# Performance work log

Measured on AMD Instinct MI355X. Metric: run time of the kernel, lower is better.

## Reference

```python
import jax, jax.numpy as jnp
import numpy as np
import math

IN_SIZE = 512
OUT_SIZE = 512
N_HEADS = 8
D_K = OUT_SIZE // N_HEADS  # 64
N_NTYPES = 4
N_ETYPES = 8
MAX_LEN = 240
E = 150000


def _sinusoid_table():
    # RelTemporalEncoding fixed (non-trainable) embedding table [MAX_LEN, IN_SIZE]
    position = np.arange(0.0, MAX_LEN, dtype=np.float64)[:, None]
    div_term = np.exp(np.arange(0, IN_SIZE, 2, dtype=np.float64) * -(math.log(10000.0) / IN_SIZE))
    emb = np.zeros((MAX_LEN, IN_SIZE), dtype=np.float64)
    emb[:, 0::2] = np.sin(position * div_term) / IN_SIZE ** 0.5
    emb[:, 1::2] = np.cos(position * div_term) / IN_SIZE ** 0.5
    return jnp.asarray(emb, dtype=jnp.float32)


def typed_linear(x, types, W, b=None):
    """x: [E, ..., in], types: int[E], W: [T, out, in], b: [T, out] or None.
    Small fixed loop over T types with masked accumulation (avoids gathering a
    huge [E, out, in] weight tensor)."""
    out = jnp.zeros(x.shape[:-1] + (W.shape[1],), x.dtype)
    t_exp = types.reshape((-1,) + (1,) * (x.ndim - 1))
    for t in range(W.shape[0]):
        y = jnp.einsum('...i,oi->...o', x, W[t])
        if b is not None:
            y = y + b[t]
        out = out + jnp.where(t_exp == t, y, jnp.zeros((), x.dtype))
    return out


def setup_inputs() -> dict:
    key = jax.random.key(0)
    ks = jax.random.split(key, 12)
    xavier = lambda k, shape, fan_in, fan_out: jax.random.uniform(
        k, shape, jnp.float32, -1.0, 1.0) * math.sqrt(6.0 / (fan_in + fan_out))
    inp = {
        'h_s': jax.random.normal(ks[0], (E, IN_SIZE), jnp.float32),
        'Q_t': jax.random.normal(ks[1], (E, N_HEADS, D_K), jnp.float32),
        'etype': jax.random.randint(ks[2], (E,), 0, N_ETYPES),
        'tau_s': jax.random.randint(ks[3], (E,), 0, N_NTYPES),
        'dt': jax.random.randint(ks[4], (E,), 0, MAX_LEN),
        # RelTemporalEncoding params
        'emb': _sinusoid_table(),  # fixed, non-trainable
        'lin_W': xavier(ks[5], (IN_SIZE, IN_SIZE), IN_SIZE, IN_SIZE),
        'lin_b': jnp.zeros((IN_SIZE,), jnp.float32),
        # TypedLinear params (xavier_uniform like the torch code)
        'K_W': xavier(ks[6], (N_NTYPES, OUT_SIZE, IN_SIZE), IN_SIZE, OUT_SIZE),
        'K_b': jnp.zeros((N_NTYPES, OUT_SIZE), jnp.float32),
        'V_W': xavier(ks[7], (N_NTYPES, OUT_SIZE, IN_SIZE), IN_SIZE, OUT_SIZE),
        'V_b': jnp.zeros((N_NTYPES, OUT_SIZE), jnp.float32),
        'Watt_W': xavier(ks[8], (N_ETYPES, D_K, D_K), D_K, D_K),
        'Wmsg_W': xavier(ks[9], (N_ETYPES, D_K, D_K), D_K, D_K),
        'mu': jnp.ones((N_ETYPES, N_HEADS), jnp.float32),
    }
    return inp


def reference(h_s, Q_t, etype, tau_s, dt, emb, lin_W, lin_b,
              K_W, K_b, V_W, V_b, Watt_W, Wmsg_W, mu):
    n_edges = h_s.shape[0]
    # RelTemporalEncoding: x + Linear(emb[t])
    h_hat = h_s + emb[dt] @ lin_W.T + lin_b  # [E, in]
    # Typed K/V projections by source node type
    K_s = typed_linear(h_hat, tau_s, K_W, K_b).reshape(n_edges, N_HEADS, D_K)
    V_s = typed_linear(h_hat, tau_s, V_W, V_b).reshape(n_edges, N_HEADS, D_K)
    # Typed per-edge-type transforms
    M = typed_linear(V_s, etype, Wmsg_W)          # [E, H, d_k]
    att_head_k = typed_linear(K_s, etype, Watt_W)  # [E, H, d_k]
    att_head = (Q_t * att_head_k).sum(-1)          # [E, H]
    att_head = att_head * mu[etype] / D_K ** 0.5
    return att_head, M
```

## Files before the change

### kernel.cpp

```cpp
#include <hip/hip_runtime.h>
#include <hip/hip_bf16.h>
#include <stdint.h>

#define E_N 150000
#define IN 512
#define MAXLEN 240

#define PT 150528
#define PE 150528
#define NTILE_T 1176

typedef __attribute__((ext_vector_type(8))) short short8;
typedef __attribute__((ext_vector_type(4))) short short4v;
typedef __attribute__((ext_vector_type(4))) float f32x4;

#define OFF_R    0UL
#define OFF_WC   491520UL
#define OFF_BIAS 4685824UL
#define OFF_CNT  4702208UL
#define OFF_PT   4702464UL
#define OFF_PE   5304576UL
#define OFF_KS   5906688UL

static __device__ __forceinline__ short f2bf(float f) {
  union { float f; uint32_t u; } v; v.f = f;
  uint32_t u = v.u;
  uint32_t r = (u + 0x7fffu + ((u >> 16) & 1u)) >> 16;
  return (short)r;
}

__global__ __launch_bounds__(256) void k_rte(const float* __restrict__ emb,
    const float* __restrict__ linW, const float* __restrict__ linB,
    float* __restrict__ R) {
  __shared__ float x[IN];
  int p = blockIdx.x;
  for (int i = threadIdx.x; i < IN; i += 256) x[i] = emb[p * IN + i];
  __syncthreads();
  for (int o = threadIdx.x; o < IN; o += 256) {
    const float* w = linW + (long)o * IN;
    float s = 0.f;
#pragma unroll 4
    for (int k = 0; k < IN; k += 4) {
      float4 wv = *(const float4*)(w + k);
      s += wv.x * x[k] + wv.y * x[k + 1] + wv.z * x[k + 2] + wv.w * x[k + 3];
    }
    R[p * IN + o] = s + linB[o];
  }
}

__global__ __launch_bounds__(256) void k_cvtw(const float* __restrict__ KW,
    const float* __restrict__ VW, short* __restrict__ Wc) {
  long idx = ((long)blockIdx.x * 256 + threadIdx.x) * 4;
  int t = (int)(idx >> 19);
  int rem = (int)(idx & ((1 << 19) - 1));
  int o = rem >> 9;
  int k = rem & 511;
  const float* src = (o < 512) ? (KW + ((long)(t * 512 + o) * 512) + k)
                               : (VW + ((long)(t * 512 + (o - 512)) * 512) + k);
  float4 v = *(const float4*)src;
  short4v b;
  b.x = f2bf(v.x); b.y = f2bf(v.y); b.z = f2bf(v.z); b.w = f2bf(v.w);
  *(short4v*)(Wc + idx) = b;
}

__global__ __launch_bounds__(256) void k_cvtb(const float* __restrict__ Kb,
    const float* __restrict__ Vb, float* __restrict__ biasC) {
  int idx = blockIdx.x * 256 + threadIdx.x;
  int t = idx >> 10;
  int o = idx & 1023;
  biasC[idx] = (o < 512) ? Kb[t * 512 + o] : Vb[t * 512 + (o - 512)];
}

__global__ __launch_bounds__(256) void k_hist(const int* __restrict__ tau,
    const int* __restrict__ et, int* __restrict__ cnt) {
  __shared__ int l[12];
  if (threadIdx.x < 12) l[threadIdx.x] = 0;
  __syncthreads();
  int e = blockIdx.x * 256 + threadIdx.x;
  if (e < E_N) {
    atomicAdd(&l[tau[e]], 1);
    atomicAdd(&l[4 + et[e]], 1);
  }
  __syncthreads();
  if (threadIdx.x < 12) atomicAdd(&cnt[threadIdx.x], l[threadIdx.x]);
}

__global__ void k_bases(int* c) {
  int b = 0;
  for (int t = 0; t < 4; t++) { c[12 + t] = b; b += ((c[t] + 127) >> 7) << 7; }
  b = 0;
  for (int g = 0; g < 8; g++) { c[16 + g] = b; b += ((c[4 + g] + 63) >> 6) << 6; }
  for (int i = 24; i < 36; i++) c[i] = 0;
}

__global__ __launch_bounds__(256) void k_scatter(const int* __restrict__ tau,
    const int* __restrict__ et, int* __restrict__ c,
    int* __restrict__ permT, int* __restrict__ permE) {
  __shared__ int lc[12], lbase[12];
  if (threadIdx.x < 12) lc[threadIdx.x] = 0;
  __syncthreads();
  int e = blockIdx.x * 256 + threadIdx.x;
  bool v = e < E_N;
  int t = 0, g = 0, pt = 0, pe = 0;
  if (v) {
    t = tau[e]; g = et[e];
    pt = atomicAdd(&lc[t], 1);
    pe = atomicAdd(&lc[4 + g], 1);
  }
  __syncthreads();
  if (threadIdx.x < 12) {
    int n = lc[threadIdx.x];
    int base = 0;
    if (n > 0) {
      if (threadIdx.x < 4) base = atomicAdd(&c[24 + threadIdx.x], n);
      else                 base = atomicAdd(&c[28 + (threadIdx.x - 4)], n);
    }
    lbase[threadIdx.x] = base;
  }
  __syncthreads();
  if (v) {
    permT[c[12 + t] + lbase[t] + pt] = e;
    permE[c[16 + g] + lbase[4 + g] + pe] = e;
  }
}

__global__ __launch_bounds__(256) void k_hhat(const float* __restrict__ hs,
    const float* __restrict__ R, const int* __restrict__ dt,
    char* __restrict__ out) {
  int tid = threadIdx.x;
  long e = (long)blockIdx.x * 16 + (tid >> 4);
  int sub = tid & 15;
  const float* hp = hs + e * 512 + sub * 32;
  const float* rp = R + (long)dt[e] * 512 + sub * 32;
  short* op = (short*)(out + e * 2048) + sub * 32;
#pragma unroll
  for (int j = 0; j < 4; j++) {
    float4 h0 = *(const float4*)(hp + j * 8);
    float4 h1 = *(const float4*)(hp + j * 8 + 4);
    float4 r0 = *(const float4*)(rp + j * 8);
    float4 r1 = *(const float4*)(rp + j * 8 + 4);
    short8 o;
    o[0] = f2bf(h0.x + r0.x); o[1] = f2bf(h0.y + r0.y);
    o[2] = f2bf(h0.z + r0.z); o[3] = f2bf(h0.w + r0.w);
    o[4] = f2bf(h1.x + r1.x); o[5] = f2bf(h1.y + r1.y);
    o[6] = f2bf(h1.z + r1.z); o[7] = f2bf(h1.w + r1.w);
    *(short8*)(op + j * 8) = o;
  }
}

__global__ __launch_bounds__(256, 4) void k_gemm(
    const char* __restrict__ hhat,
    const int* __restrict__ tau,
    const short* __restrict__ Wc, const float* __restrict__ biasC,
    const int* __restrict__ perm,
    short* __restrict__ Ks, float* Mout) {
  __shared__ short sA[4096];
  __shared__ short sB[4096];
  __shared__ int eRow[128];
  __shared__ int metaT;
  int tid = threadIdx.x;
  int l = (blockIdx.x & 7) * NTILE_T + (blockIdx.x >> 3);
  int ttile = l >> 3, ctile = l & 7;
  int m0 = ttile * 128;
  if (tid < 128) eRow[tid] = perm[m0 + tid];
  if (tid == 0) {
    int e0 = perm[m0];
    metaT = (e0 >= 0) ? tau[e0] : -1;
  }
  __syncthreads();
  int t = metaT;
  if (t < 0) return;
  int n0 = ctile * 128;

  int lane = tid & 63;
  int w = tid >> 6;
  int wm = w >> 1, wn = w & 1;

  int rS = w * 32 + (lane >> 2);
  int cS = lane & 3;
  int e0r = eRow[rS];      if (e0r < 0) e0r = 0;
  int e1r = eRow[rS + 16]; if (e1r < 0) e1r = 0;
  int ch0 = (cS - (rS >> 1)) & 3;
  int ch1 = (cS - ((rS + 16) >> 1)) & 3;
  const char* srcA0 = hhat + (size_t)e0r * 2048 + ch0 * 16;
  const char* srcA1 = hhat + (size_t)e1r * 2048 + ch1 * 16;
  const char* wcb = (const char*)(Wc + ((size_t)t * 1024 + n0) * 512);
  const char* srcB0 = wcb + (size_t)rS * 1024 + ch0 * 16;
  const char* srcB1 = wcb + (size_t)(rS + 16) * 1024 + ch1 * 16;
  char* dA0 = (char*)sA + w * 2048;
  char* dA1 = (char*)sA + w * 2048 + 1024;
  char* dB0 = (char*)sB + w * 2048;
  char* dB1 = (char*)sB + w * 2048 + 1024;

  int aRow = wm * 64 + (lane & 15);
  int aOff = aRow * 64 + ((((lane >> 4) + (aRow >> 1)) & 3) << 4);
  int bRow = wn * 64 + (lane & 15);
  int bOff = bRow * 64 + ((((lane >> 4) + (bRow >> 1)) & 3) << 4);

  f32x4 acc[4][4] = {};
#pragma unroll
  for (int kk = 0; kk < 16; kk++) {
    __syncthreads();
    __builtin_amdgcn_global_load_lds((const uint32_t*)(srcA0 + kk * 64), (uint32_t*)dA0, 16, 0, 0);
    __builtin_amdgcn_global_load_lds((const uint32_t*)(srcA1 + kk * 64), (uint32_t*)dA1, 16, 0, 0);
    __builtin_amdgcn_global_load_lds((const uint32_t*)(srcB0 + kk * 64), (uint32_t*)dB0, 16, 0, 0);
    __builtin_amdgcn_global_load_lds((const uint32_t*)(srcB1 + kk * 64), (uint32_t*)dB1, 16, 0, 0);
    __syncthreads();
    short8 a[4], b[4];
#pragma unroll
    for (int mi = 0; mi < 4; mi++)
      a[mi] = *(const short8*)((const char*)sA + aOff + mi * 1024);
#pragma unroll
    for (int ni = 0; ni < 4; ni++)
      b[ni] = *(const short8*)((const char*)sB + bOff + ni * 1024);
#pragma unroll
    for (int mi = 0; mi < 4; mi++)
#pragma unroll
      for (int ni = 0; ni < 4; ni++)
        acc[mi][ni] = __builtin_amdgcn_mfma_f32_16x16x32_bf16(a[mi], b[ni], acc[mi][ni], 0, 0, 0);
  }

  int l15 = lane & 15;
  int rbase = (lane >> 4) * 4;
  bool isK = ctile < 4;
  float bias[4];
#pragma unroll
  for (int ni = 0; ni < 4; ni++)
    bias[ni] = biasC[t * 1024 + n0 + wn * 64 + ni * 16 + l15];
#pragma unroll
  for (int mi = 0; mi < 4; mi++) {
#pragma unroll
    for (int r = 0; r < 4; r++) {
      int row = wm * 64 + mi * 16 + rbase + r;
      int e = eRow[row];
      if (e < 0) continue;
      if (isK) {
        short* kd = Ks + (size_t)e * 512 + n0 + wn * 64;
#pragma unroll
        for (int ni = 0; ni < 4; ni++)
          kd[ni * 16 + l15] = f2bf(acc[mi][ni][r] + bias[ni]);
      } else {
        short* vd = (short*)((char*)Mout + (size_t)e * 2048 + 1024) + (n0 - 512) + wn * 64;
#pragma unroll
        for (int ni = 0; ni < 4; ni++)
          vd[ni * 16 + l15] = f2bf(acc[mi][ni][r] + bias[ni]);
      }
    }
  }
}

__global__ __launch_bounds__(512, 1) void k_msg(
    const int* __restrict__ perm, const int* __restrict__ et,
    const float* __restrict__ WmsgW, float* Mout) {
  __shared__ short Wm[64][68];
  __shared__ int eArr[64];
  __shared__ int metaG;
  int tid = threadIdx.x;
  int m0 = blockIdx.x * 64;
  if (tid < 64) eArr[tid] = perm[m0 + tid];
  if (tid == 0) {
    int e0 = perm[m0];
    metaG = (e0 >= 0) ? et[e0] : -1;
  }
  __syncthreads();
  int g = metaG;
  if (g < 0) return;
  for (int i = tid; i < 4096; i += 512)
    Wm[i >> 6][i & 63] = f2bf(WmsgW[(long)g * 4096 + i]);
  __syncthreads();

  int lane = tid & 63;
  int wv = tid >> 6;
  int wvBase = wv * 64;
  int l15 = lane & 15;
  int lk8 = (lane >> 4) * 8;
  int rbase = (lane >> 4) * 4;

  short8 av[4][2];
#pragma unroll
  for (int mi = 0; mi < 4; mi++) {
    int lr = wvBase + mi * 16 + l15;
    int e = eArr[lr >> 3]; if (e < 0) e = 0;
    const short* vp = (const short*)((const char*)Mout + (size_t)e * 2048 + 1024)
                      + (lr & 7) * 64 + lk8;
    av[mi][0] = *(const short8*)vp;
    av[mi][1] = *(const short8*)(vp + 32);
  }
  short8 bm[4][2];
#pragma unroll
  for (int ni = 0; ni < 4; ni++)
#pragma unroll
    for (int kk = 0; kk < 2; kk++)
      bm[ni][kk] = *(const short8*)&Wm[ni * 16 + l15][kk * 32 + lk8];
  f32x4 accM[4][4] = {};
#pragma unroll
  for (int kk = 0; kk < 2; kk++)
#pragma unroll
    for (int mi = 0; mi < 4; mi++)
#pragma unroll
      for (int ni = 0; ni < 4; ni++)
        accM[mi][ni] = __builtin_amdgcn_mfma_f32_16x16x32_bf16(av[mi][kk], bm[ni][kk], accM[mi][ni], 0, 0, 0);
#pragma unroll
  for (int mi = 0; mi < 4; mi++) {
#pragma unroll
    for (int r = 0; r < 4; r++) {
      int lr = wvBase + mi * 16 + rbase + r;
      int e = eArr[lr >> 3];
      if (e < 0) continue;
      int h = lr & 7;
#pragma unroll
      for (int ni = 0; ni < 4; ni++)
        Mout[(long)e * 512 + h * 64 + ni * 16 + l15] = accM[mi][ni][r];
    }
  }
}

__global__ __launch_bounds__(512, 1) void k_att(
    const int* __restrict__ perm, const int* __restrict__ et,
    const float* __restrict__ WattW, const float* __restrict__ Qt,
    const float* __restrict__ mu, const short* __restrict__ Ks,
    float* __restrict__ attOut) {
  __shared__ short Wa[64][68];
  __shared__ float muL[8];
  __shared__ int eArr[64];
  __shared__ int metaG;
  int tid = threadIdx.x;
  int m0 = blockIdx.x * 64;
  if (tid < 64) eArr[tid] = perm[m0 + tid];
  if (tid == 0) {
    int e0 = perm[m0];
    metaG = (e0 >= 0) ? et[e0] : -1;
  }
  __syncthreads();
  int g = metaG;
  if (g < 0) return;
  for (int i = tid; i < 4096; i += 512)
    Wa[i >> 6][i & 63] = f2bf(WattW[(long)g * 4096 + i]);
  if (tid < 8) muL[tid] = mu[g * 8 + tid];
  __syncthreads();

  int lane = tid & 63;
  int wv = tid >> 6;
  int wvBase = wv * 64;
  int l15 = lane & 15;
  int lk8 = (lane >> 4) * 8;
  int rbase = (lane >> 4) * 4;

  short8 ak[4][2];
#pragma unroll
  for (int mi = 0; mi < 4; mi++) {
    int lr = wvBase + mi * 16 + l15;
    int e = eArr[lr >> 3]; if (e < 0) e = 0;
    const short* kp = Ks + (size_t)e * 512 + (lr & 7) * 64 + lk8;
    ak[mi][0] = *(const short8*)kp;
    ak[mi][1] = *(const short8*)(kp + 32);
  }
  short8 ba[4][2];
#pragma unroll
  for (int ni = 0; ni < 4; ni++)
#pragma unroll
    for (int kk = 0; kk < 2; kk++)
      ba[ni][kk] = *(const short8*)&Wa[ni * 16 + l15][kk * 32 + lk8];
  f32x4 accA[4][4] = {};
#pragma unroll
  for (int kk = 0; kk < 2; kk++)
#pragma unroll
    for (int mi = 0; mi < 4; mi++)
#pragma unroll
      for (int ni = 0; ni < 4; ni++)
        accA[mi][ni] = __builtin_amdgcn_mfma_f32_16x16x32_bf16(ak[mi][kk], ba[ni][kk], accA[mi][ni], 0, 0, 0);
#pragma unroll
  for (int mi = 0; mi < 4; mi++) {
#pragma unroll
    for (int r = 0; r < 4; r++) {
      int lr = wvBase + mi * 16 + rbase + r;
      int e = eArr[lr >> 3];
      if (e < 0) continue;
      int h = lr & 7;
      const float* qp = Qt + ((long)e * 8 + h) * 64 + l15;
      float s = 0.f;
#pragma unroll
      for (int ni = 0; ni < 4; ni++)
        s += qp[ni * 16] * accA[mi][ni][r];
      s += __shfl_xor(s, 1);
      s += __shfl_xor(s, 2);
      s += __shfl_xor(s, 4);
      s += __shfl_xor(s, 8);
      if (l15 == 0) attOut[(long)e * 8 + h] = s * muL[h] * 0.125f;
    }
  }
}

extern "C" void kernel_launch(void* const* d_in, const int* in_sizes, int n_in,
                              void* d_out, int out_size, void* d_ws, size_t ws_size,
                              hipStream_t stream) {
  const float* hs    = (const float*)d_in[0];
  const float* Qt    = (const float*)d_in[1];
  const int*   et    = (const int*)d_in[2];
  const int*   tau   = (const int*)d_in[3];
  const int*   dt    = (const int*)d_in[4];
  const float* emb   = (const float*)d_in[5];
  const float* linW  = (const float*)d_in[6];
  const float* linB  = (const float*)d_in[7];
  const float* KW    = (const float*)d_in[8];
  const float* Kb    = (const float*)d_in[9];
  const float* VW    = (const float*)d_in[10];
  const float* Vb    = (const float*)d_in[11];
  const float* WattW = (const float*)d_in[12];
  const float* WmsgW = (const float*)d_in[13];
  const float* mu    = (const float*)d_in[14];

  char* ws = (char*)d_ws;
  float* R     = (float*)(ws + OFF_R);
  short* Wc    = (short*)(ws + OFF_WC);
  float* biasC = (float*)(ws + OFF_BIAS);
  int*   cnt   = (int*)(ws + OFF_CNT);
  int*   permT = (int*)(ws + OFF_PT);
  int*   permE = (int*)(ws + OFF_PE);
  short* Ks    = (short*)(ws + OFF_KS);

  float* attOut = (float*)d_out;
  float* Mout   = (float*)d_out + (long)E_N * 8;

  hipMemsetAsync(cnt, 0, 64 * sizeof(int), stream);
  hipMemsetAsync(permT, 0xFF, PT * sizeof(int), stream);
  hipMemsetAsync(permE, 0xFF, PE * sizeof(int), stream);

  k_rte<<<240, 256, 0, stream>>>(emb, linW, linB, R);
  k_cvtw<<<2048, 256, 0, stream>>>(KW, VW, Wc);
  k_cvtb<<<16, 256, 0, stream>>>(Kb, Vb, biasC);
  k_hist<<<(E_N + 255) / 256, 256, 0, stream>>>(tau, et, cnt);
  k_bases<<<1, 1, 0, stream>>>(cnt);
  k_scatter<<<(E_N + 255) / 256, 256, 0, stream>>>(tau, et, cnt, permT, permE);
  k_hhat<<<E_N / 16, 256, 0, stream>>>(hs, R, dt, (char*)Mout);
  k_gemm<<<NTILE_T * 8, 256, 0, stream>>>((const char*)Mout, tau, Wc, biasC, permT, Ks, Mout);
  k_msg<<<PE / 64, 512, 0, stream>>>(permE, et, WmsgW, Mout);
  k_att<<<PE / 64, 512, 0, stream>>>(permE, et, WattW, Qt, mu, Ks, attOut);
}
```

Baseline: 693.3 us.

## Fold per-edge-type transforms into typed K/V weights and precompute temporal term

Pre-multiplies the per-edge-type Watt/Wmsg matrices into the per-node-type K/V weights, giving 32 combined (tau, etype) weight sets. Edges are bucketed by that pair. The temporal-encoding contribution is precomputed as a 240-row table per pair, so the main GEMM consumes h_s directly, converting fp32 to bf16 on the fly. The attention dot product with Q and the M store are fused into the GEMM epilogue. This removes the h_hat materialisation, the intermediate K/V buffers and the separate message and attention kernels. The cost is more padding from 32 buckets, a large RW table read per edge in the epilogue, and different rounding from bf16 combined weights.

```diff
diff --git a/kernel.cpp b/kernel.cpp
--- a/kernel.cpp
+++ b/kernel.cpp
@@ -6,21 +6,19 @@
 #define IN 512
 #define MAXLEN 240
 
-#define PT 150528
-#define PE 150528
-#define NTILE_T 1176
+#define PPERM 154112
+#define NTILE2 1204
+#define GRID_GEMM (NTILE2 * 8)
 
 typedef __attribute__((ext_vector_type(8))) short short8;
-typedef __attribute__((ext_vector_type(4))) short short4v;
 typedef __attribute__((ext_vector_type(4))) float f32x4;
 
-#define OFF_R    0UL
-#define OFF_WC   491520UL
-#define OFF_BIAS 4685824UL
-#define OFF_CNT  4702208UL
-#define OFF_PT   4702464UL
-#define OFF_PE   5304576UL
-#define OFF_KS   5906688UL
+#define OFF_RB   0UL
+#define OFF_W2   245760UL
+#define OFF_B2   33800192UL
+#define OFF_RW   33931264UL
+#define OFF_CNT  65388544UL
+#define OFF_PERM 65389056UL
 
 static __device__ __forceinline__ short f2bf(float f) {
   union { float f; uint32_t u; } v; v.f = f;
@@ -29,9 +27,15 @@
   return (short)r;
 }
 
+static __device__ __forceinline__ uint32_t pk2(float a, float b) {
+  union { __hip_bfloat162 h; uint32_t u; } v;
+  v.h = __float22bfloat162_rn(make_float2(a, b));
+  return v.u;
+}
+
 __global__ __launch_bounds__(256) void k_rte(const float* __restrict__ emb,
     const float* __restrict__ linW, const float* __restrict__ linB,
-    float* __restrict__ R) {
+    short* __restrict__ Rbf) {
   __shared__ float x[IN];
   int p = blockIdx.x;
   for (int i = threadIdx.x; i < IN; i += 256) x[i] = emb[p * IN + i];
@@ -44,147 +48,76 @@
       float4 wv = *(const float4*)(w + k);
       s += wv.x * x[k] + wv.y * x[k + 1] + wv.z * x[k + 2] + wv.w * x[k + 3];
     }
-    R[p * IN + o] = s + linB[o];
-  }
-}
-
-__global__ __launch_bounds__(256) void k_cvtw(const float* __restrict__ KW,
-    const float* __restrict__ VW, short* __restrict__ Wc) {
-  long idx = ((long)blockIdx.x * 256 + threadIdx.x) * 4;
-  int t = (int)(idx >> 19);
-  int rem = (int)(idx & ((1 << 19) - 1));
-  int o = rem >> 9;
-  int k = rem & 511;
-  const float* src = (o < 512) ? (KW + ((long)(t * 512 + o) * 512) + k)
-                               : (VW + ((long)(t * 512 + (o - 512)) * 512) + k);
-  float4 v = *(const float4*)src;
-  short4v b;
-  b.x = f2bf(v.x); b.y = f2bf(v.y); b.z = f2bf(v.z); b.w = f2bf(v.w);
-  *(short4v*)(Wc + idx) = b;
-}
-
-__global__ __launch_bounds__(256) void k_cvtb(const float* __restrict__ Kb,
-    const float* __restrict__ Vb, float* __restrict__ biasC) {
-  int idx = blockIdx.x * 256 + threadIdx.x;
-  int t = idx >> 10;
-  int o = idx & 1023;
-  biasC[idx] = (o < 512) ? Kb[t * 512 + o] : Vb[t * 512 + (o - 512)];
-}
-
-__global__ __launch_bounds__(256) void k_hist(const int* __restrict__ tau,
-    const int* __restrict__ et, int* __restrict__ cnt) {
-  __shared__ int l[12];
-  if (threadIdx.x < 12) l[threadIdx.x] = 0;
-  __syncthreads();
-  int e = blockIdx.x * 256 + threadIdx.x;
-  if (e < E_N) {
-    atomicAdd(&l[tau[e]], 1);
-    atomicAdd(&l[4 + et[e]], 1);
-  }
-  __syncthreads();
-  if (threadIdx.x < 12) atomicAdd(&cnt[threadIdx.x], l[threadIdx.x]);
-}
-
-__global__ void k_bases(int* c) {
-  int b = 0;
-  for (int t = 0; t < 4; t++) { c[12 + t] = b; b += ((c[t] + 127) >> 7) << 7; }
-  b = 0;
-  for (int g = 0; g < 8; g++) { c[16 + g] = b; b += ((c[4 + g] + 63) >> 6) << 6; }
-  for (int i = 24; i < 36; i++) c[i] = 0;
-}
-
-__global__ __launch_bounds__(256) void k_scatter(const int* __restrict__ tau,
-    const int* __restrict__ et, int* __restrict__ c,
-    int* __restrict__ permT, int* __restrict__ permE) {
-  __shared__ int lc[12], lbase[12];
-  if (threadIdx.x < 12) lc[threadIdx.x] = 0;
-  __syncthreads();
-  int e = blockIdx.x * 256 + threadIdx.x;
-  bool v = e < E_N;
-  int t = 0, g = 0, pt = 0, pe = 0;
-  if (v) {
-    t = tau[e]; g = et[e];
-    pt = atomicAdd(&lc[t], 1);
-    pe = atomicAdd(&lc[4 + g], 1);
-  }
-  __syncthreads();
-  if (threadIdx.x < 12) {
-    int n = lc[threadIdx.x];
-    int base = 0;
-    if (n > 0) {
-      if (threadIdx.x < 4) base = atomicAdd(&c[24 + threadIdx.x], n);
-      else                 base = atomicAdd(&c[28 + (threadIdx.x - 4)], n);
-    }
-    lbase[threadIdx.x] = base;
-  }
-  __syncthreads();
-  if (v) {
-    permT[c[12 + t] + lbase[t] + pt] = e;
-    permE[c[16 + g] + lbase[4 + g] + pe] = e;
-  }
-}
-
-__global__ __launch_bounds__(256) void k_hhat(const float* __restrict__ hs,
-    const float* __restrict__ R, const int* __restrict__ dt,
-    char* __restrict__ out) {
+    Rbf[p * IN + o] = f2bf(s + linB[o]);
+  }
+}
+
+__global__ __launch_bounds__(256) void k_wpair(
+    const float* __restrict__ WattW, const float* __restrict__ WmsgW,
+    const float* __restrict__ KW, const float* __restrict__ VW,
+    const float* __restrict__ Kb, const float* __restrict__ Vb,
+    short* __restrict__ W2, float* __restrict__ B2) {
+  __shared__ float Tl[64][65];
+  int blk = blockIdx.x;
+  int p = blk >> 4, s = blk & 15;
+  int t = p >> 3, g = p & 7;
+  bool kside = s < 8;
+  int h = kside ? s : s - 8;
+  const float* T = (kside ? WattW : WmsgW) + (size_t)g * 4096;
+  const float* S = (kside ? KW : VW) + ((size_t)t * 512 + h * 64) * 512;
+  const float* bsrc = (kside ? Kb : Vb) + t * 512 + h * 64;
   int tid = threadIdx.x;
-  long e = (long)blockIdx.x * 16 + (tid >> 4);
-  int sub = tid & 15;
-  const float* hp = hs + e * 512 + sub * 32;
-  const float* rp = R + (long)dt[e] * 512 + sub * 32;
-  short* op = (short*)(out + e * 2048) + sub * 32;
-#pragma unroll
-  for (int j = 0; j < 4; j++) {
-    float4 h0 = *(const float4*)(hp + j * 8);
-    float4 h1 = *(const float4*)(hp + j * 8 + 4);
-    float4 r0 = *(const float4*)(rp + j * 8);
-    float4 r1 = *(const float4*)(rp + j * 8 + 4);
-    short8 o;
-    o[0] = f2bf(h0.x + r0.x); o[1] = f2bf(h0.y + r0.y);
-    o[2] = f2bf(h0.z + r0.z); o[3] = f2bf(h0.w + r0.w);
-    o[4] = f2bf(h1.x + r1.x); o[5] = f2bf(h1.y + r1.y);
-    o[6] = f2bf(h1.z + r1.z); o[7] = f2bf(h1.w + r1.w);
-    *(short8*)(op + j * 8) = o;
-  }
-}
-
-__global__ __launch_bounds__(256, 4) void k_gemm(
-    const char* __restrict__ hhat,
-    const int* __restrict__ tau,
-    const short* __restrict__ Wc, const float* __restrict__ biasC,
-    const int* __restrict__ perm,
-    short* __restrict__ Ks, float* Mout) {
+  for (int i = tid; i < 4096; i += 256) Tl[i >> 6][i & 63] = T[i];
+  __syncthreads();
+  int op = tid & 63, iq = tid >> 6;
+  size_t obase = ((size_t)p * 1024 + (kside ? 0 : 512) + h * 64 + op) * 512;
+  for (int i8 = 0; i8 < 16; i8++) {
+    int i0 = iq * 128 + i8 * 8;
+    float a0 = 0, a1 = 0, a2 = 0, a3 = 0, a4 = 0, a5 = 0, a6 = 0, a7 = 0;
+    const float* sp0 = S + i0;
+#pragma unroll 8
+    for (int j = 0; j < 64; j++) {
+      float tv = Tl[op][j];
+      const float* sp = sp0 + j * 512;
+      float4 s0 = *(const float4*)sp;
+      float4 s1 = *(const float4*)(sp + 4);
+      a0 += tv * s0.x; a1 += tv * s0.y; a2 += tv * s0.z; a3 += tv * s0.w;
+      a4 += tv * s1.x; a5 += tv * s1.y; a6 += tv * s1.z; a7 += tv * s1.w;
+    }
+    short8 o8;
+    o8[0] = f2bf(a0); o8[1] = f2bf(a1); o8[2] = f2bf(a2); o8[3] = f2bf(a3);
+    o8[4] = f2bf(a4); o8[5] = f2bf(a5); o8[6] = f2bf(a6); o8[7] = f2bf(a7);
+    *(short8*)(W2 + obase + i0) = o8;
+  }
+  if (tid < 64) {
+    float b = 0;
+#pragma unroll 8
+    for (int j = 0; j < 64; j++) b += Tl[tid][j] * bsrc[j];
+    B2[p * 1024 + (kside ? 0 : 512) + h * 64 + tid] = b;
+  }
+}
+
+__global__ __launch_bounds__(256, 4) void k_rw2(
+    const short* __restrict__ Rbf, const short* __restrict__ W2,
+    const float* __restrict__ B2, float* __restrict__ RW) {
   __shared__ short sA[4096];
   __shared__ short sB[4096];
-  __shared__ int eRow[128];
-  __shared__ int metaT;
   int tid = threadIdx.x;
-  int l = (blockIdx.x & 7) * NTILE_T + (blockIdx.x >> 3);
-  int ttile = l >> 3, ctile = l & 7;
-  int m0 = ttile * 128;
-  if (tid < 128) eRow[tid] = perm[m0 + tid];
-  if (tid == 0) {
-    int e0 = perm[m0];
-    metaT = (e0 >= 0) ? tau[e0] : -1;
-  }
-  __syncthreads();
-  int t = metaT;
-  if (t < 0) return;
+  int bid = blockIdx.x;
+  int p = bid >> 4, rt = (bid >> 3) & 1, ctile = bid & 7;
   int n0 = ctile * 128;
-
-  int lane = tid & 63;
-  int w = tid >> 6;
-  int wm = w >> 1, wn = w & 1;
+  int r0 = rt * 128;
+
+  int lane = tid & 63, w = tid >> 6, wm = w >> 1, wn = w & 1;
 
   int rS = w * 32 + (lane >> 2);
   int cS = lane & 3;
-  int e0r = eRow[rS];      if (e0r < 0) e0r = 0;
-  int e1r = eRow[rS + 16]; if (e1r < 0) e1r = 0;
   int ch0 = (cS - (rS >> 1)) & 3;
   int ch1 = (cS - ((rS + 16) >> 1)) & 3;
-  const char* srcA0 = hhat + (size_t)e0r * 2048 + ch0 * 16;
-  const char* srcA1 = hhat + (size_t)e1r * 2048 + ch1 * 16;
-  const char* wcb = (const char*)(Wc + ((size_t)t * 1024 + n0) * 512);
+  const char* rbb = (const char*)Rbf;
+  const char* srcA0 = rbb + (size_t)(r0 + rS) * 1024 + ch0 * 16;
+  const char* srcA1 = rbb + (size_t)(r0 + rS + 16) * 1024 + ch1 * 16;
+  const char* wcb = (const char*)(W2 + ((size_t)p * 1024 + n0) * 512);
   const char* srcB0 = wcb + (size_t)rS * 1024 + ch0 * 16;
   const char* srcB1 = wcb + (size_t)(rS + 16) * 1024 + ch1 * 16;
   char* dA0 = (char*)sA + w * 2048;
@@ -222,171 +155,195 @@
 
   int l15 = lane & 15;
   int rbase = (lane >> 4) * 4;
-  bool isK = ctile < 4;
   float bias[4];
 #pragma unroll
   for (int ni = 0; ni < 4; ni++)
-    bias[ni] = biasC[t * 1024 + n0 + wn * 64 + ni * 16 + l15];
+    bias[ni] = B2[p * 1024 + n0 + wn * 64 + ni * 16 + l15];
 #pragma unroll
   for (int mi = 0; mi < 4; mi++) {
 #pragma unroll
     for (int r = 0; r < 4; r++) {
-      int row = wm * 64 + mi * 16 + rbase + r;
-      int e = eRow[row];
-      if (e < 0) continue;
-      if (isK) {
-        short* kd = Ks + (size_t)e * 512 + n0 + wn * 64;
-#pragma unroll
-        for (int ni = 0; ni < 4; ni++)
-          kd[ni * 16 + l15] = f2bf(acc[mi][ni][r] + bias[ni]);
-      } else {
-        short* vd = (short*)((char*)Mout + (size_t)e * 2048 + 1024) + (n0 - 512) + wn * 64;
-#pragma unroll
-        for (int ni = 0; ni < 4; ni++)
-          vd[ni * 16 + l15] = f2bf(acc[mi][ni][r] + bias[ni]);
-      }
-    }
-  }
-}
-
-__global__ __launch_bounds__(512, 1) void k_msg(
-    const int* __restrict__ perm, const int* __restrict__ et,
-    const float* __restrict__ WmsgW, float* Mout) {
-  __shared__ short Wm[64][68];
-  __shared__ int eArr[64];
-  __shared__ int metaG;
+      int row = r0 + wm * 64 + mi * 16 + rbase + r;
+      if (row >= MAXLEN) continue;
+      float* dst = RW + ((size_t)p * 240 + row) * 1024 + n0 + wn * 64;
+#pragma unroll
+      for (int ni = 0; ni < 4; ni++)
+        dst[ni * 16 + l15] = acc[mi][ni][r] + bias[ni];
+    }
+  }
+}
+
+__global__ __launch_bounds__(256) void k_hist(const int* __restrict__ tau,
+    const int* __restrict__ et, int* __restrict__ cnt) {
+  __shared__ int l[32];
+  if (threadIdx.x < 32) l[threadIdx.x] = 0;
+  __syncthreads();
+  int e = blockIdx.x * 256 + threadIdx.x;
+  if (e < E_N) atomicAdd(&l[tau[e] * 8 + et[e]], 1);
+  __syncthreads();
+  if (threadIdx.x < 32) atomicAdd(&cnt[threadIdx.x], l[threadIdx.x]);
+}
+
+__global__ void k_bases(int* c) {
+  int b = 0;
+  for (int p = 0; p < 32; p++) {
+    c[32 + p] = b;
+    b += ((c[p] + 127) >> 7) << 7;
+    c[64 + p] = 0;
+  }
+}
+
+__global__ __launch_bounds__(256) void k_scatter(const int* __restrict__ tau,
+    const int* __restrict__ et, int* __restrict__ c, int* __restrict__ perm) {
+  __shared__ int lc[32], lbase[32];
+  if (threadIdx.x < 32) lc[threadIdx.x] = 0;
+  __syncthreads();
+  int e = blockIdx.x * 256 + threadIdx.x;
+  bool v = e < E_N;
+  int cls = 0, pos = 0;
+  if (v) {
+    cls = tau[e] * 8 + et[e];
+    pos = atomicAdd(&lc[cls], 1);
+  }
+  __syncthreads();
+  if (threadIdx.x < 32) {
+    int n = lc[threadIdx.x];
+    lbase[threadIdx.x] = (n > 0) ? atomicAdd(&c[64 + threadIdx.x], n) : 0;
+  }
+  __syncthreads();
+  if (v) perm[c[32 + cls] + lbase[cls] + pos] = e;
+}
+
+__global__ __launch_bounds__(256, 4) void k_gemm(
+    const float* __restrict__ hs, const int* __restrict__ dt,
+    const int* __restrict__ tau, const int* __restrict__ et,
+    const short* __restrict__ W2, const float* __restrict__ RW,
+    const float* __restrict__ Qt, const float* __restrict__ mu,
+    const int* __restrict__ perm,
+    float* __restrict__ Mout, float* __restrict__ attOut) {
+  __shared__ short sA[128][40];
+  __shared__ short sB[4096];
+  __shared__ int eRow[128];
+  __shared__ int dtRow[128];
+  __shared__ int metaP;
   int tid = threadIdx.x;
-  int m0 = blockIdx.x * 64;
-  if (tid < 64) eArr[tid] = perm[m0 + tid];
+  int l = (blockIdx.x & 7) * NTILE2 + (blockIdx.x >> 3);
+  int ttile = l >> 3, ctile = l & 7;
+  int m0 = ttile * 128;
+  if (tid < 128) {
+    int e = perm[m0 + tid];
+    eRow[tid] = e;
+    dtRow[tid] = (e >= 0) ? dt[e] : 0;
+  }
   if (tid == 0) {
     int e0 = perm[m0];
-    metaG = (e0 >= 0) ? et[e0] : -1;
-  }
-  __syncthreads();
-  int g = metaG;
-  if (g < 0) return;
-  for (int i = tid; i < 4096; i += 512)
-    Wm[i >> 6][i & 63] = f2bf(WmsgW[(long)g * 4096 + i]);
-  __syncthreads();
-
-  int lane = tid & 63;
-  int wv = tid >> 6;
-  int wvBase = wv * 64;
+    metaP = (e0 >= 0) ? (tau[e0] * 8 + et[e0]) : -1;
+  }
+  __syncthreads();
+  int p = metaP;
+  if (p < 0) return;
+  int n0 = ctile * 128;
+
+  int lane = tid & 63, w = tid >> 6, wm = w >> 1, wn = w & 1;
+
+  int arow = tid >> 1;
+  int ahalf = tid & 1;
+  long aE = eRow[arow]; if (aE < 0) aE = 0;
+  const float* asrc = hs + aE * 512 + ahalf * 16;
+
+  int rS = w * 32 + (lane >> 2);
+  int cS = lane & 3;
+  int ch0 = (cS - (rS >> 1)) & 3;
+  int ch1 = (cS - ((rS + 16) >> 1)) & 3;
+  const char* wcb = (const char*)(W2 + ((size_t)p * 1024 + n0) * 512);
+  const char* srcB0 = wcb + (size_t)rS * 1024 + ch0 * 16;
+  const char* srcB1 = wcb + (size_t)(rS + 16) * 1024 + ch1 * 16;
+  char* dB0 = (char*)sB + w * 2048;
+  char* dB1 = (char*)sB + w * 2048 + 1024;
+
+  int aRowF = wm * 64 + (lane & 15);
+  int lk8 = (lane >> 4) * 8;
+  int bRow = wn * 64 + (lane & 15);
+  int bOff = bRow * 64 + ((((lane >> 4) + (bRow >> 1)) & 3) << 4);
+
+  f32x4 acc[4][4] = {};
+  float4 pf0 = *(const float4*)(asrc);
+  float4 pf1 = *(const float4*)(asrc + 4);
+  float4 pf2 = *(const float4*)(asrc + 8);
+  float4 pf3 = *(const float4*)(asrc + 12);
+#pragma unroll
+  for (int kk = 0; kk < 16; kk++) {
+    __syncthreads();
+    union { short8 s; uint32_t u[4]; } w0, w1;
+    w0.u[0] = pk2(pf0.x, pf0.y); w0.u[1] = pk2(pf0.z, pf0.w);
+    w0.u[2] = pk2(pf1.x, pf1.y); w0.u[3] = pk2(pf1.z, pf1.w);
+    w1.u[0] = pk2(pf2.x, pf2.y); w1.u[1] = pk2(pf2.z, pf2.w);
+    w1.u[2] = pk2(pf3.x, pf3.y); w1.u[3] = pk2(pf3.z, pf3.w);
+    *(short8*)&sA[arow][ahalf * 16] = w0.s;
+    *(short8*)&sA[arow][ahalf * 16 + 8] = w1.s;
+    __builtin_amdgcn_global_load_lds((const uint32_t*)(srcB0 + kk * 64), (uint32_t*)dB0, 16, 0, 0);
+    __builtin_amdgcn_global_load_lds((const uint32_t*)(srcB1 + kk * 64), (uint32_t*)dB1, 16, 0, 0);
+    if (kk < 15) {
+      const float* np = asrc + (kk + 1) * 32;
+      pf0 = *(const float4*)(np);
+      pf1 = *(const float4*)(np + 4);
+      pf2 = *(const float4*)(np + 8);
+      pf3 = *(const float4*)(np + 12);
+    }
+    __syncthreads();
+    short8 a[4], b[4];
+#pragma unroll
+    for (int mi = 0; mi < 4; mi++)
+      a[mi] = *(const short8*)&sA[aRowF + mi * 16][lk8];
+#pragma unroll
+    for (int ni = 0; ni < 4; ni++)
+      b[ni] = *(const short8*)((const char*)sB + bOff + ni * 1024);
+#pragma unroll
+    for (int mi = 0; mi < 4; mi++)
+#pragma unroll
+      for (int ni = 0; ni < 4; ni++)
+        acc[mi][ni] = __builtin_amdgcn_mfma_f32_16x16x32_bf16(a[mi], b[ni], acc[mi][ni], 0, 0, 0);
+  }
+
   int l15 = lane & 15;
-  int lk8 = (lane >> 4) * 8;
   int rbase = (lane >> 4) * 4;
-
-  short8 av[4][2];
-#pragma unroll
-  for (int mi = 0; mi < 4; mi++) {
-    int lr = wvBase + mi * 16 + l15;
-    int e = eArr[lr >> 3]; if (e < 0) e = 0;
-    const short* vp = (const short*)((const char*)Mout + (size_t)e * 2048 + 1024)
-                      + (lr & 7) * 64 + lk8;
-    av[mi][0] = *(const short8*)vp;
-    av[mi][1] = *(const short8*)(vp + 32);
-  }
-  short8 bm[4][2];
-#pragma unroll
-  for (int ni = 0; ni < 4; ni++)
-#pragma unroll
-    for (int kk = 0; kk < 2; kk++)
-      bm[ni][kk] = *(const short8*)&Wm[ni * 16 + l15][kk * 32 + lk8];
-  f32x4 accM[4][4] = {};
-#pragma unroll
-  for (int kk = 0; kk < 2; kk++)
-#pragma unroll
-    for (int mi = 0; mi < 4; mi++)
-#pragma unroll
-      for (int ni = 0; ni < 4; ni++)
-        accM[mi][ni] = __builtin_amdgcn_mfma_f32_16x16x32_bf16(av[mi][kk], bm[ni][kk], accM[mi][ni], 0, 0, 0);
-#pragma unroll
-  for (int mi = 0; mi < 4; mi++) {
-#pragma unroll
-    for (int r = 0; r < 4; r++) {
-      int lr = wvBase + mi * 16 + rbase + r;
-      int e = eArr[lr >> 3];
-      if (e < 0) continue;
-      int h = lr & 7;
-#pragma unroll
-      for (int ni = 0; ni < 4; ni++)
-        Mout[(long)e * 512 + h * 64 + ni * 16 + l15] = accM[mi][ni][r];
-    }
-  }
-}
-
-__global__ __launch_bounds__(512, 1) void k_att(
-    const int* __restrict__ perm, const int* __restrict__ et,
-    const float* __restrict__ WattW, const float* __restrict__ Qt,
-    const float* __restrict__ mu, const short* __restrict__ Ks,
-    float* __restrict__ attOut) {
-  __shared__ short Wa[64][68];
-  __shared__ float muL[8];
-  __shared__ int eArr[64];
-  __shared__ int metaG;
-  int tid = threadIdx.x;
-  int m0 = blockIdx.x * 64;
-  if (tid < 64) eArr[tid] = perm[m0 + tid];
-  if (tid == 0) {
-    int e0 = perm[m0];
-    metaG = (e0 >= 0) ? et[e0] : -1;
-  }
-  __syncthreads();
-  int g = metaG;
-  if (g < 0) return;
-  for (int i = tid; i < 4096; i += 512)
-    Wa[i >> 6][i & 63] = f2bf(WattW[(long)g * 4096 + i]);
-  if (tid < 8) muL[tid] = mu[g * 8 + tid];
-  __syncthreads();
-
-  int lane = tid & 63;
-  int wv = tid >> 6;
-  int wvBase = wv * 64;
-  int l15 = lane & 15;
-  int lk8 = (lane >> 4) * 8;
-  int rbase = (lane >> 4) * 4;
-
-  short8 ak[4][2];
-#pragma unroll
-  for (int mi = 0; mi < 4; mi++) {
-    int lr = wvBase + mi * 16 + l15;
-    int e = eArr[lr >> 3]; if (e < 0) e = 0;
-    const short* kp = Ks + (size_t)e * 512 + (lr & 7) * 64 + lk8;
-    ak[mi][0] = *(const short8*)kp;
-    ak[mi][1] = *(const short8*)(kp + 32);
-  }
-  short8 ba[4][2];
-#pragma unroll
-  for (int ni = 0; ni < 4; ni++)
-#pragma unroll
-    for (int kk = 0; kk < 2; kk++)
-      ba[ni][kk] = *(const short8*)&Wa[ni * 16 + l15][kk * 32 + lk8];
-  f32x4 accA[4][4] = {};
-#pragma unroll
-  for (int kk = 0; kk < 2; kk++)
-#pragma unroll
-    for (int mi = 0; mi < 4; mi++)
-#pragma unroll
-      for (int ni = 0; ni < 4; ni++)
-        accA[mi][ni] = __builtin_amdgcn_mfma_f32_16x16x32_bf16(ak[mi][kk], ba[ni][kk], accA[mi][ni], 0, 0, 0);
-#pragma unroll
-  for (int mi = 0; mi < 4; mi++) {
-#pragma unroll
-    for (int r = 0; r < 4; r++) {
-      int lr = wvBase + mi * 16 + rbase + r;
-      int e = eArr[lr >> 3];
-      if (e < 0) continue;
-      int h = lr & 7;
-      const float* qp = Qt + ((long)e * 8 + h) * 64 + l15;
-      float s = 0.f;
-#pragma unroll
-      for (int ni = 0; ni < 4; ni++)
-        s += qp[ni * 16] * accA[mi][ni][r];
-      s += __shfl_xor(s, 1);
-      s += __shfl_xor(s, 2);
-      s += __shfl_xor(s, 4);
-      s += __shfl_xor(s, 8);
-      if (l15 == 0) attOut[(long)e * 8 + h] = s * muL[h] * 0.125f;
+  if (ctile < 4) {
+    int h = ctile * 2 + wn;
+    float muv = mu[(p & 7) * 8 + h] * 0.125f;
+#pragma unroll
+    for (int mi = 0; mi < 4; mi++) {
+#pragma unroll
+      for (int r = 0; r < 4; r++) {
+        int row = wm * 64 + mi * 16 + rbase + r;
+        int e = eRow[row];
+        if (e < 0) continue;
+        const float* rw = RW + ((size_t)p * 240 + dtRow[row]) * 1024 + n0 + wn * 64;
+        const float* qp = Qt + (size_t)e * 512 + h * 64;
+        float s = 0.f;
+#pragma unroll
+        for (int ni = 0; ni < 4; ni++)
+          s += qp[ni * 16 + l15] * (acc[mi][ni][r] + rw[ni * 16 + l15]);
+        s += __shfl_xor(s, 1);
+        s += __shfl_xor(s, 2);
+        s += __shfl_xor(s, 4);
+        s += __shfl_xor(s, 8);
+        if (l15 == 0) attOut[(size_t)e * 8 + h] = s * muv;
+      }
+    }
+  } else {
+#pragma unroll
+    for (int mi = 0; mi < 4; mi++) {
+#pragma unroll
+      for (int r = 0; r < 4; r++) {
+        int row = wm * 64 + mi * 16 + rbase + r;
+        int e = eRow[row];
+        if (e < 0) continue;
+        const float* rw = RW + ((size_t)p * 240 + dtRow[row]) * 1024 + n0 + wn * 64;
+        float* md = Mout + (size_t)e * 512 + (n0 - 512) + wn * 64;
+#pragma unroll
+        for (int ni = 0; ni < 4; ni++)
+          md[ni * 16 + l15] = acc[mi][ni][r] + rw[ni * 16 + l15];
+      }
     }
   }
 }
@@ -411,29 +368,24 @@
   const float* mu    = (const float*)d_in[14];
 
   char* ws = (char*)d_ws;
-  float* R     = (float*)(ws + OFF_R);
-  short* Wc    = (short*)(ws + OFF_WC);
-  float* biasC = (float*)(ws + OFF_BIAS);
-  int*   cnt   = (int*)(ws + OFF_CNT);
-  int*   permT = (int*)(ws + OFF_PT);
-  int*   permE = (int*)(ws + OFF_PE);
-  short* Ks    = (short*)(ws + OFF_KS);
+  short* Rbf  = (short*)(ws + OFF_RB);
+  short* W2   = (short*)(ws + OFF_W2);
+  float* B2   = (float*)(ws + OFF_B2);
+  float* RW   = (float*)(ws + OFF_RW);
+  int*   cnt  = (int*)(ws + OFF_CNT);
+  int*   perm = (int*)(ws + OFF_PERM);
 
   float* attOut = (float*)d_out;
   float* Mout   = (float*)d_out + (long)E_N * 8;
 
-  hipMemsetAsync(cnt, 0, 64 * sizeof(int), stream);
-  hipMemsetAsync(permT, 0xFF, PT * sizeof(int), stream);
-  hipMemsetAsync(permE, 0xFF, PE * sizeof(int), stream);
-
-  k_rte<<<240, 256, 0, stream>>>(emb, linW, linB, R);
-  k_cvtw<<<2048, 256, 0, stream>>>(KW, VW, Wc);
-  k_cvtb<<<16, 256, 0, stream>>>(Kb, Vb, biasC);
+  hipMemsetAsync(cnt, 0, 128 * sizeof(int), stream);
+  hipMemsetAsync(perm, 0xFF, PPERM * sizeof(int), stream);
+
+  k_rte<<<240, 256, 0, stream>>>(emb, linW, linB, Rbf);
+  k_wpair<<<512, 256, 0, stream>>>(WattW, WmsgW, KW, VW, Kb, Vb, W2, B2);
   k_hist<<<(E_N + 255) / 256, 256, 0, stream>>>(tau, et, cnt);
   k_bases<<<1, 1, 0, stream>>>(cnt);
-  k_scatter<<<(E_N + 255) / 256, 256, 0, stream>>>(tau, et, cnt, permT, permE);
-  k_hhat<<<E_N / 16, 256, 0, stream>>>(hs, R, dt, (char*)Mout);
-  k_gemm<<<NTILE_T * 8, 256, 0, stream>>>((const char*)Mout, tau, Wc, biasC, permT, Ks, Mout);
-  k_msg<<<PE / 64, 512, 0, stream>>>(permE, et, WmsgW, Mout);
-  k_att<<<PE / 64, 512, 0, stream>>>(permE, et, WattW, Qt, mu, Ks, attOut);
-}
+  k_scatter<<<(E_N + 255) / 256, 256, 0, stream>>>(tau, et, cnt, perm);
+  k_rw2<<<512, 256, 0, stream>>>(Rbf, W2, B2, RW);
+  k_gemm<<<GRID_GEMM, 256, 0, stream>>>(hs, dt, tau, et, W2, RW, Qt, mu, perm, Mout, attOut);
+}
```

Measured after the change: 713.9 us. +3.0%, slower.
